# Optimization experiments

Measured on AMD Instinct MI355X. Metric: run time of the kernel, lower is better.

Reference implementation:

```python
import jax, jax.numpy as jnp
import numpy as np

N = 8_388_608
T_MAX = 4096


def setup_inputs() -> dict:
    key = jax.random.key(0)
    k1, k2, k3 = jax.random.split(key, 3)
    risk = jax.random.normal(k1, (N,), dtype=jnp.float32)
    time = jax.random.randint(k2, (N,), 0, T_MAX, dtype=jnp.int64)
    event = jax.random.randint(k3, (N,), 0, 2, dtype=jnp.int64)
    return {"risk": risk, "time": time, "event": event}


def reference(risk, time, event):
    # Sort descending by time (matches torch.argsort(time, descending=True)).
    order = jnp.argsort(-time)
    r = risk[order]            # [N] risk sorted by descending time
    t = time[order]            # [N]
    e = event[order] > 0       # [N] bool

    n = r.shape[0]
    # Cumulative (prefix) logsumexp over descending-sorted risks.
    # At-risk set for time t is exactly the prefix ending at the LAST index
    # of t's tie group, so log_denom(group) = clse[last_idx_of_group].
    clse = jax.lax.associative_scan(jnp.logaddexp, r)  # [N]

    # Last index of each contiguous tie block (times equal => contiguous after sort).
    is_last = jnp.concatenate([t[:-1] != t[1:], jnp.ones((1,), dtype=bool)])
    idx = jnp.arange(n)
    cand = jnp.where(is_last, idx, n)          # non-last positions -> sentinel
    last_idx = jax.lax.cummin(cand, axis=0, reverse=True)  # min over j >= i

    log_denom = clse[last_idx]                 # [N] per-sample group denominator

    # nll = -sum_groups(sum_{events in group} risk  -  d_group * log_denom)
    #     =  sum_{i: event_i} (log_denom_i - risk_i)
    nll = jnp.sum(jnp.where(e, log_denom - r, jnp.float32(0.0)))

    has_events = jnp.sum(event > 0) > 0
    return jnp.where(has_events, nll, jnp.float32(0.0))
```

## Files before the change

kernel.cpp:

```cpp
#include <hip/hip_runtime.h>

#define TMAX 4096
#define ABLOCKS 512
#define ATHREADS 1024
#define PERTHREAD_V4 4

#define SCALE_F 1048576.0f
#define INV_SCALE (1.0 / 1048576.0)
#define SUM_MASK 0xFFFFFFFFFFFFULL
#define CNT_SHIFT 48

#define RB 32
#define RS 32

__global__ __launch_bounds__(ATHREADS, 8) void coxph_hist_fixed(
    const float* __restrict__ risk, const int* __restrict__ time_,
    const int* __restrict__ event,
    float* __restrict__ psum, unsigned short* __restrict__ pcnt,
    float* __restrict__ pevr)
{
    __shared__ unsigned long long s_acc[TMAX];
    __shared__ float s_evr[ATHREADS / 64];

    const int tid = threadIdx.x;
    #pragma unroll
    for (int k = 0; k < TMAX / ATHREADS; ++k) s_acc[tid + k * ATHREADS] = 0ull;
    __syncthreads();

    const float4* r4 = (const float4*)risk;
    const int4*   t4 = (const int4*)time_;
    const int4*   e4 = (const int4*)event;

    const int base = blockIdx.x * ATHREADS + tid;
    const int STRIDE4 = ABLOCKS * ATHREADS;

    float4 r[PERTHREAD_V4]; int4 t[PERTHREAD_V4]; int4 e[PERTHREAD_V4];
    #pragma unroll
    for (int k = 0; k < PERTHREAD_V4; ++k) {
        const int i = base + k * STRIDE4;
        r[k] = r4[i]; t[k] = t4[i]; e[k] = e4[i];
    }

    float evr = 0.f;
    #pragma unroll
    for (int k = 0; k < PERTHREAD_V4; ++k) {
        {
            unsigned long long pk =
                (unsigned long long)(__expf(r[k].x) * SCALE_F + 0.5f)
                | ((unsigned long long)(unsigned)e[k].x << CNT_SHIFT);
            atomicAdd(&s_acc[t[k].x & (TMAX - 1)], pk);
            evr += e[k].x ? r[k].x : 0.f;
        }
        {
            unsigned long long pk =
                (unsigned long long)(__expf(r[k].y) * SCALE_F + 0.5f)
                | ((unsigned long long)(unsigned)e[k].y << CNT_SHIFT);
            atomicAdd(&s_acc[t[k].y & (TMAX - 1)], pk);
            evr += e[k].y ? r[k].y : 0.f;
        }
        {
            unsigned long long pk =
                (unsigned long long)(__expf(r[k].z) * SCALE_F + 0.5f)
                | ((unsigned long long)(unsigned)e[k].z << CNT_SHIFT);
            atomicAdd(&s_acc[t[k].z & (TMAX - 1)], pk);
            evr += e[k].z ? r[k].z : 0.f;
        }
        {
            unsigned long long pk =
                (unsigned long long)(__expf(r[k].w) * SCALE_F + 0.5f)
                | ((unsigned long long)(unsigned)e[k].w << CNT_SHIFT);
            atomicAdd(&s_acc[t[k].w & (TMAX - 1)], pk);
            evr += e[k].w ? r[k].w : 0.f;
        }
    }

    #pragma unroll
    for (int off = 32; off > 0; off >>= 1) evr += __shfl_down(evr, off);
    const int lane = tid & 63, wave = tid >> 6;
    if (lane == 0) s_evr[wave] = evr;
    __syncthreads();

    float*          ps = psum + (size_t)blockIdx.x * TMAX;
    unsigned short* pc = pcnt + (size_t)blockIdx.x * TMAX;
    #pragma unroll
    for (int k = 0; k < TMAX / ATHREADS; ++k) {
        const int i = tid + k * ATHREADS;
        unsigned long long v = s_acc[i];
        ps[i] = (float)((double)(v & SUM_MASK) * INV_SCALE);
        pc[i] = (unsigned short)(v >> CNT_SHIFT);
    }
    if (tid == 0) {
        float tot = 0.f;
        for (int w = 0; w < ATHREADS / 64; ++w) tot += s_evr[w];
        pevr[blockIdx.x] = tot;
    }
}

__global__ __launch_bounds__(ATHREADS, 8) void coxph_hist_generic(
    const float* __restrict__ risk, const int* __restrict__ time_,
    const int* __restrict__ event,
    float* __restrict__ psum, unsigned short* __restrict__ pcnt,
    float* __restrict__ pevr, int n)
{
    __shared__ unsigned long long s_acc[TMAX];
    __shared__ float s_evr[ATHREADS / 64];

    const int tid = threadIdx.x;
    #pragma unroll
    for (int k = 0; k < TMAX / ATHREADS; ++k) s_acc[tid + k * ATHREADS] = 0ull;
    __syncthreads();

    float evr = 0.f;
    const int stride = gridDim.x * ATHREADS;
    for (int i = blockIdx.x * ATHREADS + tid; i < n; i += stride) {
        float rv = risk[i];
        int   ev = event[i];
        unsigned long long pk =
            (unsigned long long)(__expf(rv) * SCALE_F + 0.5f)
            | ((unsigned long long)(unsigned)ev << CNT_SHIFT);
        atomicAdd(&s_acc[time_[i] & (TMAX - 1)], pk);
        evr += ev ? rv : 0.f;
    }

    #pragma unroll
    for (int off = 32; off > 0; off >>= 1) evr += __shfl_down(evr, off);
    const int lane = tid & 63, wave = tid >> 6;
    if (lane == 0) s_evr[wave] = evr;
    __syncthreads();

    float*          ps = psum + (size_t)blockIdx.x * TMAX;
    unsigned short* pc = pcnt + (size_t)blockIdx.x * TMAX;
    #pragma unroll
    for (int k = 0; k < TMAX / ATHREADS; ++k) {
        const int i = tid + k * ATHREADS;
        unsigned long long v = s_acc[i];
        ps[i] = (float)((double)(v & SUM_MASK) * INV_SCALE);
        pc[i] = (unsigned short)(v >> CNT_SHIFT);
    }
    if (tid == 0) {
        float tot = 0.f;
        for (int w = 0; w < ATHREADS / 64; ++w) tot += s_evr[w];
        pevr[blockIdx.x] = tot;
    }
}

__global__ __launch_bounds__(1024) void coxph_reduce(
    const float* __restrict__ psum, const unsigned short* __restrict__ pcnt,
    float* __restrict__ bsum, unsigned* __restrict__ bcnt)
{
    __shared__ float    ls[RS * RB];
    __shared__ unsigned lc[RS * RB];

    const int t = threadIdx.x;
    const int j = t & (RB - 1);
    const int s = t >> 5;
    const int bucket = blockIdx.x * RB + j;

    float sum = 0.f; unsigned cnt = 0u;
    #pragma unroll
    for (int k = 0; k < ABLOCKS / RS; ++k) {
        const int row = s * (ABLOCKS / RS) + k;
        sum += psum[(size_t)row * TMAX + bucket];
        cnt += pcnt[(size_t)row * TMAX + bucket];
    }
    ls[t] = sum; lc[t] = cnt;
    __syncthreads();

    #pragma unroll
    for (int h = RS / 2; h >= 1; h >>= 1) {
        if (s < h) { ls[t] += ls[t + h * RB]; lc[t] += lc[t + h * RB]; }
        __syncthreads();
    }
    if (s == 0) { bsum[bucket] = ls[j]; bcnt[bucket] = lc[j]; }
}

__global__ __launch_bounds__(1024) void coxph_finalize(
    const float* __restrict__ bsum, const unsigned* __restrict__ bcnt,
    const float* __restrict__ pevr, int nevr, float* __restrict__ out)
{
    __shared__ float    s_wsum[16];
    __shared__ double   s_dacc[16];
    __shared__ unsigned s_cacc[16];

    const int tid = threadIdx.x;
    const int lane = tid & 63, wave = tid >> 6;

    const int j0 = 4 * tid;
    float v0 = bsum[TMAX - 1 - j0];
    float v1 = bsum[TMAX - 2 - j0];
    float v2 = bsum[TMAX - 3 - j0];
    float v3 = bsum[TMAX - 4 - j0];
    float p0 = v0, p1 = p0 + v1, p2 = p1 + v2, p3 = p2 + v3;

    float t_incl = p3;
    #pragma unroll
    for (int off = 1; off < 64; off <<= 1) {
        float u = __shfl_up(t_incl, off);
        if (lane >= off) t_incl += u;
    }
    if (lane == 63) s_wsum[wave] = t_incl;
    __syncthreads();
    if (tid == 0) {
        float acc = 0.f;
        for (int w = 0; w < 16; ++w) { float x = s_wsum[w]; s_wsum[w] = acc; acc += x; }
    }
    __syncthreads();
    const float excl = (t_incl - p3) + s_wsum[wave];

    double acc = 0.0;
    unsigned ctot = 0u;
    unsigned c0 = bcnt[TMAX - 1 - j0];
    unsigned c1 = bcnt[TMAX - 2 - j0];
    unsigned c2 = bcnt[TMAX - 3 - j0];
    unsigned c3 = bcnt[TMAX - 4 - j0];
    if (c0) { acc += (double)c0 * (double)logf(excl + p0); ctot += c0; }
    if (c1) { acc += (double)c1 * (double)logf(excl + p1); ctot += c1; }
    if (c2) { acc += (double)c2 * (double)logf(excl + p2); ctot += c2; }
    if (c3) { acc += (double)c3 * (double)logf(excl + p3); ctot += c3; }

    if (tid < nevr) acc -= (double)pevr[tid];

    #pragma unroll
    for (int off = 32; off > 0; off >>= 1) {
        acc  += __shfl_down(acc, off);
        ctot += __shfl_down(ctot, off);
    }
    if (lane == 0) { s_dacc[wave] = acc; s_cacc[wave] = ctot; }
    __syncthreads();
    if (tid == 0) {
        double a = 0.0; unsigned c = 0u;
        for (int w = 0; w < 16; ++w) { a += s_dacc[w]; c += s_cacc[w]; }
        out[0] = c ? (float)a : 0.0f;
    }
}

extern "C" void kernel_launch(void* const* d_in, const int* in_sizes, int n_in,
                              void* d_out, int out_size, void* d_ws, size_t ws_size,
                              hipStream_t stream)
{
    const float* risk  = (const float*)d_in[0];
    const int*   time_ = (const int*)d_in[1];
    const int*   event = (const int*)d_in[2];
    float* out = (float*)d_out;
    const int n = in_sizes[0];

    char* ws = (char*)d_ws;
    const size_t psum_bytes = (size_t)ABLOCKS * TMAX * sizeof(float);
    const size_t pcnt_bytes = (size_t)ABLOCKS * TMAX * sizeof(unsigned short);
    size_t off = 0;
    float*          psum = (float*)(ws + off);          off += psum_bytes;
    unsigned short* pcnt = (unsigned short*)(ws + off); off += pcnt_bytes;
    float*          pevr = (float*)(ws + off);          off += ABLOCKS * sizeof(float);
    float*          bsum = (float*)(ws + off);          off += TMAX * sizeof(float);
    unsigned*       bcnt = (unsigned*)(ws + off);       off += TMAX * sizeof(unsigned);

    if (ws_size >= off) {
        if (n == ABLOCKS * ATHREADS * 4 * PERTHREAD_V4) {
            coxph_hist_fixed<<<ABLOCKS, ATHREADS, 0, stream>>>(
                risk, time_, event, psum, pcnt, pevr);
        } else {
            coxph_hist_generic<<<ABLOCKS, ATHREADS, 0, stream>>>(
                risk, time_, event, psum, pcnt, pevr, n);
        }
        coxph_reduce<<<TMAX / RB, RS * RB, 0, stream>>>(psum, pcnt, bsum, bcnt);
        coxph_finalize<<<1, 1024, 0, stream>>>(bsum, bcnt, pevr, ABLOCKS, out);
    } else {
        float*    fb_sum = (float*)ws;
        unsigned short* fb_cnt = (unsigned short*)(ws + TMAX * sizeof(float));
        float*    fb_evr = (float*)(ws + TMAX * (sizeof(float) + sizeof(unsigned short)));
        float*    fb_bsum = fb_sum;
        coxph_hist_generic<<<1, ATHREADS, 0, stream>>>(
            risk, time_, event, fb_sum, fb_cnt, fb_evr, n);
        unsigned* fb_bcnt = (unsigned*)(ws + TMAX * (sizeof(float) + sizeof(unsigned short))
                                        + sizeof(float));
        struct Conv { };
        coxph_finalize<<<1, 1024, 0, stream>>>(fb_bsum, fb_bcnt, fb_evr, 1, out);
    }
}
```

Before: 125.9 us.

## Pack partial histograms as fp16 sum plus count, fuse reduce and finalize

Each histogram block now writes one 32-bit word per bucket, an fp16 partial sum in the low half and the event count in the high half, instead of separate float and ushort arrays. The separate reduce and finalize kernels become one kernel: a global atomic counter lets the last reduce block run the prefix-logsumexp finalize, which removes a launch. The reduce tiling changes to 64 buckets by 16 row-slices. This shrinks intermediate traffic and launch overhead, but fp16 partial sums lose precision and the last-block handoff relies on threadfence ordering.

```diff
diff --git a/kernel.cpp b/kernel.cpp
--- a/kernel.cpp
+++ b/kernel.cpp
@@ -1,4 +1,5 @@
 #include <hip/hip_runtime.h>
+#include <hip/hip_fp16.h>
 
 #define TMAX 4096
 #define ABLOCKS 512
@@ -6,23 +7,25 @@
 #define PERTHREAD_V4 4
 
 #define SCALE_F 1048576.0f
-#define INV_SCALE (1.0 / 1048576.0)
+#define INV_SCALE 9.5367431640625e-07f
 #define SUM_MASK 0xFFFFFFFFFFFFULL
 #define CNT_SHIFT 48
 
-#define RB 32
-#define RS 32
+#define RB 64
+#define RS 16
+#define RBLOCKS (TMAX / RB)
 
 __global__ __launch_bounds__(ATHREADS, 8) void coxph_hist_fixed(
     const float* __restrict__ risk, const int* __restrict__ time_,
     const int* __restrict__ event,
-    float* __restrict__ psum, unsigned short* __restrict__ pcnt,
-    float* __restrict__ pevr)
+    unsigned* __restrict__ ppack, float* __restrict__ pevr,
+    unsigned* __restrict__ done)
 {
     __shared__ unsigned long long s_acc[TMAX];
     __shared__ float s_evr[ATHREADS / 64];
 
     const int tid = threadIdx.x;
+    if (blockIdx.x == 0 && tid == 0) *done = 0u;
     #pragma unroll
     for (int k = 0; k < TMAX / ATHREADS; ++k) s_acc[tid + k * ATHREADS] = 0ull;
     __syncthreads();
@@ -45,30 +48,26 @@
     #pragma unroll
     for (int k = 0; k < PERTHREAD_V4; ++k) {
         {
-            unsigned long long pk =
-                (unsigned long long)(__expf(r[k].x) * SCALE_F + 0.5f)
-                | ((unsigned long long)(unsigned)e[k].x << CNT_SHIFT);
+            unsigned lo = (unsigned)(__expf(r[k].x) * SCALE_F + 0.5f);
+            unsigned long long pk = ((unsigned long long)(unsigned)e[k].x << CNT_SHIFT) | lo;
             atomicAdd(&s_acc[t[k].x & (TMAX - 1)], pk);
             evr += e[k].x ? r[k].x : 0.f;
         }
         {
-            unsigned long long pk =
-                (unsigned long long)(__expf(r[k].y) * SCALE_F + 0.5f)
-                | ((unsigned long long)(unsigned)e[k].y << CNT_SHIFT);
+            unsigned lo = (unsigned)(__expf(r[k].y) * SCALE_F + 0.5f);
+            unsigned long long pk = ((unsigned long long)(unsigned)e[k].y << CNT_SHIFT) | lo;
             atomicAdd(&s_acc[t[k].y & (TMAX - 1)], pk);
             evr += e[k].y ? r[k].y : 0.f;
         }
         {
-            unsigned long long pk =
-                (unsigned long long)(__expf(r[k].z) * SCALE_F + 0.5f)
-                | ((unsigned long long)(unsigned)e[k].z << CNT_SHIFT);
+            unsigned lo = (unsigned)(__expf(r[k].z) * SCALE_F + 0.5f);
+            unsigned long long pk = ((unsigned long long)(unsigned)e[k].z << CNT_SHIFT) | lo;
             atomicAdd(&s_acc[t[k].z & (TMAX - 1)], pk);
             evr += e[k].z ? r[k].z : 0.f;
         }
         {
-            unsigned long long pk =
-                (unsigned long long)(__expf(r[k].w) * SCALE_F + 0.5f)
-                | ((unsigned long long)(unsigned)e[k].w << CNT_SHIFT);
+            unsigned lo = (unsigned)(__expf(r[k].w) * SCALE_F + 0.5f);
+            unsigned long long pk = ((unsigned long long)(unsigned)e[k].w << CNT_SHIFT) | lo;
             atomicAdd(&s_acc[t[k].w & (TMAX - 1)], pk);
             evr += e[k].w ? r[k].w : 0.f;
         }
@@ -80,14 +79,15 @@
     if (lane == 0) s_evr[wave] = evr;
     __syncthreads();
 
-    float*          ps = psum + (size_t)blockIdx.x * TMAX;
-    unsigned short* pc = pcnt + (size_t)blockIdx.x * TMAX;
+    unsigned* pp = ppack + (size_t)blockIdx.x * TMAX;
     #pragma unroll
     for (int k = 0; k < TMAX / ATHREADS; ++k) {
         const int i = tid + k * ATHREADS;
         unsigned long long v = s_acc[i];
-        ps[i] = (float)((double)(v & SUM_MASK) * INV_SCALE);
-        pc[i] = (unsigned short)(v >> CNT_SHIFT);
+        float s = (float)(v & SUM_MASK) * INV_SCALE;
+        unsigned c = (unsigned)(v >> CNT_SHIFT);
+        unsigned hb = (unsigned)__half_as_ushort(__float2half(s));
+        pp[i] = (c << 16) | hb;
     }
     if (tid == 0) {
         float tot = 0.f;
@@ -99,13 +99,14 @@
 __global__ __launch_bounds__(ATHREADS, 8) void coxph_hist_generic(
     const float* __restrict__ risk, const int* __restrict__ time_,
     const int* __restrict__ event,
-    float* __restrict__ psum, unsigned short* __restrict__ pcnt,
-    float* __restrict__ pevr, int n)
+    unsigned* __restrict__ ppack, float* __restrict__ pevr,
+    unsigned* __restrict__ done, int n)
 {
     __shared__ unsigned long long s_acc[TMAX];
     __shared__ float s_evr[ATHREADS / 64];
 
     const int tid = threadIdx.x;
+    if (blockIdx.x == 0 && tid == 0) *done = 0u;
     #pragma unroll
     for (int k = 0; k < TMAX / ATHREADS; ++k) s_acc[tid + k * ATHREADS] = 0ull;
     __syncthreads();
@@ -115,9 +116,8 @@
     for (int i = blockIdx.x * ATHREADS + tid; i < n; i += stride) {
         float rv = risk[i];
         int   ev = event[i];
-        unsigned long long pk =
-            (unsigned long long)(__expf(rv) * SCALE_F + 0.5f)
-            | ((unsigned long long)(unsigned)ev << CNT_SHIFT);
+        unsigned lo = (unsigned)(__expf(rv) * SCALE_F + 0.5f);
+        unsigned long long pk = ((unsigned long long)(unsigned)ev << CNT_SHIFT) | lo;
         atomicAdd(&s_acc[time_[i] & (TMAX - 1)], pk);
         evr += ev ? rv : 0.f;
     }
@@ -128,14 +128,15 @@
     if (lane == 0) s_evr[wave] = evr;
     __syncthreads();
 
-    float*          ps = psum + (size_t)blockIdx.x * TMAX;
-    unsigned short* pc = pcnt + (size_t)blockIdx.x * TMAX;
+    unsigned* pp = ppack + (size_t)blockIdx.x * TMAX;
     #pragma unroll
     for (int k = 0; k < TMAX / ATHREADS; ++k) {
         const int i = tid + k * ATHREADS;
         unsigned long long v = s_acc[i];
-        ps[i] = (float)((double)(v & SUM_MASK) * INV_SCALE);
-        pc[i] = (unsigned short)(v >> CNT_SHIFT);
+        float s = (float)(v & SUM_MASK) * INV_SCALE;
+        unsigned c = (unsigned)(v >> CNT_SHIFT);
+        unsigned hb = (unsigned)__half_as_ushort(__float2half(s));
+        pp[i] = (c << 16) | hb;
     }
     if (tid == 0) {
         float tot = 0.f;
@@ -144,24 +145,27 @@
     }
 }
 
-__global__ __launch_bounds__(1024) void coxph_reduce(
-    const float* __restrict__ psum, const unsigned short* __restrict__ pcnt,
-    float* __restrict__ bsum, unsigned* __restrict__ bcnt)
+__global__ __launch_bounds__(1024) void coxph_reduce_finalize(
+    const unsigned* __restrict__ ppack, const float* __restrict__ pevr,
+    float* __restrict__ bsum, unsigned* __restrict__ bcnt,
+    unsigned* __restrict__ done, float* __restrict__ out)
 {
     __shared__ float    ls[RS * RB];
     __shared__ unsigned lc[RS * RB];
+    __shared__ unsigned s_last;
 
     const int t = threadIdx.x;
     const int j = t & (RB - 1);
-    const int s = t >> 5;
+    const int s = t >> 6;
     const int bucket = blockIdx.x * RB + j;
 
     float sum = 0.f; unsigned cnt = 0u;
     #pragma unroll
     for (int k = 0; k < ABLOCKS / RS; ++k) {
         const int row = s * (ABLOCKS / RS) + k;
-        sum += psum[(size_t)row * TMAX + bucket];
-        cnt += pcnt[(size_t)row * TMAX + bucket];
+        unsigned p = ppack[(size_t)row * TMAX + bucket];
+        sum += __half2float(__ushort_as_half((unsigned short)(p & 0xFFFFu)));
+        cnt += p >> 16;
     }
     ls[t] = sum; lc[t] = cnt;
     __syncthreads();
@@ -172,20 +176,23 @@
         __syncthreads();
     }
     if (s == 0) { bsum[bucket] = ls[j]; bcnt[bucket] = lc[j]; }
-}
-
-__global__ __launch_bounds__(1024) void coxph_finalize(
-    const float* __restrict__ bsum, const unsigned* __restrict__ bcnt,
-    const float* __restrict__ pevr, int nevr, float* __restrict__ out)
-{
+    __syncthreads();
+
+    if (t == 0) {
+        __threadfence();
+        unsigned old = atomicAdd(done, 1u);
+        s_last = (old == RBLOCKS - 1) ? 1u : 0u;
+    }
+    __syncthreads();
+    if (!s_last) return;
+    __threadfence();
+
     __shared__ float    s_wsum[16];
     __shared__ double   s_dacc[16];
     __shared__ unsigned s_cacc[16];
 
-    const int tid = threadIdx.x;
-    const int lane = tid & 63, wave = tid >> 6;
-
-    const int j0 = 4 * tid;
+    const int lane = t & 63, wave = t >> 6;
+    const int j0 = 4 * t;
     float v0 = bsum[TMAX - 1 - j0];
     float v1 = bsum[TMAX - 2 - j0];
     float v2 = bsum[TMAX - 3 - j0];
@@ -200,7 +207,7 @@
     }
     if (lane == 63) s_wsum[wave] = t_incl;
     __syncthreads();
-    if (tid == 0) {
+    if (t == 0) {
         float acc = 0.f;
         for (int w = 0; w < 16; ++w) { float x = s_wsum[w]; s_wsum[w] = acc; acc += x; }
     }
@@ -218,7 +225,7 @@
     if (c2) { acc += (double)c2 * (double)logf(excl + p2); ctot += c2; }
     if (c3) { acc += (double)c3 * (double)logf(excl + p3); ctot += c3; }
 
-    if (tid < nevr) acc -= (double)pevr[tid];
+    if (t < ABLOCKS) acc -= (double)pevr[t];
 
     #pragma unroll
     for (int off = 32; off > 0; off >>= 1) {
@@ -227,7 +234,7 @@
     }
     if (lane == 0) { s_dacc[wave] = acc; s_cacc[wave] = ctot; }
     __syncthreads();
-    if (tid == 0) {
+    if (t == 0) {
         double a = 0.0; unsigned c = 0u;
         for (int w = 0; w < 16; ++w) { a += s_dacc[w]; c += s_cacc[w]; }
         out[0] = c ? (float)a : 0.0f;
@@ -245,35 +252,20 @@
     const int n = in_sizes[0];
 
     char* ws = (char*)d_ws;
-    const size_t psum_bytes = (size_t)ABLOCKS * TMAX * sizeof(float);
-    const size_t pcnt_bytes = (size_t)ABLOCKS * TMAX * sizeof(unsigned short);
     size_t off = 0;
-    float*          psum = (float*)(ws + off);          off += psum_bytes;
-    unsigned short* pcnt = (unsigned short*)(ws + off); off += pcnt_bytes;
-    float*          pevr = (float*)(ws + off);          off += ABLOCKS * sizeof(float);
-    float*          bsum = (float*)(ws + off);          off += TMAX * sizeof(float);
-    unsigned*       bcnt = (unsigned*)(ws + off);       off += TMAX * sizeof(unsigned);
-
-    if (ws_size >= off) {
-        if (n == ABLOCKS * ATHREADS * 4 * PERTHREAD_V4) {
-            coxph_hist_fixed<<<ABLOCKS, ATHREADS, 0, stream>>>(
-                risk, time_, event, psum, pcnt, pevr);
-        } else {
-            coxph_hist_generic<<<ABLOCKS, ATHREADS, 0, stream>>>(
-                risk, time_, event, psum, pcnt, pevr, n);
-        }
-        coxph_reduce<<<TMAX / RB, RS * RB, 0, stream>>>(psum, pcnt, bsum, bcnt);
-        coxph_finalize<<<1, 1024, 0, stream>>>(bsum, bcnt, pevr, ABLOCKS, out);
+    unsigned* ppack = (unsigned*)(ws + off); off += (size_t)ABLOCKS * TMAX * sizeof(unsigned);
+    float*    pevr  = (float*)(ws + off);    off += ABLOCKS * sizeof(float);
+    float*    bsum  = (float*)(ws + off);    off += TMAX * sizeof(float);
+    unsigned* bcnt  = (unsigned*)(ws + off); off += TMAX * sizeof(unsigned);
+    unsigned* done  = (unsigned*)(ws + off); off += sizeof(unsigned);
+
+    if (n == ABLOCKS * ATHREADS * 4 * PERTHREAD_V4) {
+        coxph_hist_fixed<<<ABLOCKS, ATHREADS, 0, stream>>>(
+            risk, time_, event, ppack, pevr, done);
     } else {
-        float*    fb_sum = (float*)ws;
-        unsigned short* fb_cnt = (unsigned short*)(ws + TMAX * sizeof(float));
-        float*    fb_evr = (float*)(ws + TMAX * (sizeof(float) + sizeof(unsigned short)));
-        float*    fb_bsum = fb_sum;
-        coxph_hist_generic<<<1, ATHREADS, 0, stream>>>(
-            risk, time_, event, fb_sum, fb_cnt, fb_evr, n);
-        unsigned* fb_bcnt = (unsigned*)(ws + TMAX * (sizeof(float) + sizeof(unsigned short))
-                                        + sizeof(float));
-        struct Conv { };
-        coxph_finalize<<<1, 1024, 0, stream>>>(fb_bsum, fb_bcnt, fb_evr, 1, out);
-    }
-}
+        coxph_hist_generic<<<ABLOCKS, ATHREADS, 0, stream>>>(
+            risk, time_, event, ppack, pevr, done, n);
+    }
+    coxph_reduce_finalize<<<RBLOCKS, RS * RB, 0, stream>>>(
+        ppack, pevr, bsum, bcnt, done, out);
+}
```

Measured after the change: 127.0 us. About the same (+0.9%).
